# Kernel tuning notes

Hardware: AMD Instinct MI355X
Metric: run time of the kernel (lower is better)

Reference implementation:

```python
import jax, jax.numpy as jnp
import numpy as np

B, Q, S = 4, 256, 2048          # seqs, new query tokens per seq, total kv len per seq
H, KVH, D = 32, 8, 128          # query heads, kv heads (GQA), head dim
BLOCK = 16                      # paged-cache block size
NUM_BLOCKS = 640                # total blocks in the cache pool
BLOCKS_PER_SEQ = S // BLOCK     # 128


def setup_inputs() -> dict:
    key = jax.random.key(0)
    ks = jax.random.split(key, 5)
    T = B * Q
    q = jax.random.normal(ks[0], (T, H * D), jnp.float32)
    k = jax.random.normal(ks[1], (T, KVH * D), jnp.float32)
    v = jax.random.normal(ks[2], (T, KVH * D), jnp.float32)
    # pre-existing paged cache contents (context tokens already written)
    kv_cache = jax.random.normal(ks[3], (2, NUM_BLOCKS, BLOCK, KVH, D), jnp.float32)
    # assign blocks to sequences via a permutation (irregular block layout)
    perm = jax.random.permutation(ks[4], NUM_BLOCKS)[: B * BLOCKS_PER_SEQ]
    block_tables = perm.reshape(B, BLOCKS_PER_SEQ).astype(jnp.int32)
    # new tokens are the last Q positions of each sequence
    pos = jnp.arange(S - Q, S)
    slot_mapping = (block_tables[:, pos // BLOCK] * BLOCK + pos % BLOCK).reshape(-1).astype(jnp.int32)
    seq_lens = jnp.full((B,), S, jnp.int32)
    query_start_loc = (jnp.arange(B + 1) * Q).astype(jnp.int32)
    return dict(q=q, k=k, v=v, kv_cache=kv_cache, slot_mapping=slot_mapping,
                block_tables=block_tables, seq_lens=seq_lens, query_start_loc=query_start_loc)


def _paged_attention(q, k, v, kv_cache, slot_mapping, block_tables, seq_lens):
    T = q.shape[0]
    nB, _ = block_tables.shape
    _, _, block_size, kvh, d = kv_cache.shape
    h = q.shape[1] // d
    g = h // kvh                      # GQA group size
    qlen = T // nB                    # equal query lens (query_start_loc is uniform)
    scale = d ** -0.5
    # A) scatter new K/V into the flattened paged cache at slot_mapping
    kc = kv_cache[0].reshape(-1, kvh, d).at[slot_mapping].set(k.reshape(T, kvh, d))
    vc = kv_cache[1].reshape(-1, kvh, d).at[slot_mapping].set(v.reshape(T, kvh, d))
    # B) gather each sequence's kv via block_tables indirection  -> [B, S, KVH, D]
    slots = (block_tables[:, :, None] * block_size + jnp.arange(block_size)).reshape(nB, -1)
    k_seq = kc[slots]
    v_seq = vc[slots]
    s_kv = slots.shape[1]
    qh = q.reshape(nB, qlen, kvh, g, d)
    scores = jnp.einsum('bqkgd,bskd->bkgqs', qh, k_seq) * scale  # [B,KVH,G,Q,S]
    # causal mask: query qi sits at absolute pos seq_lens[b]-qlen+qi
    qpos = seq_lens[:, None] - qlen + jnp.arange(qlen)           # [B,Q]
    kpos = jnp.arange(s_kv)
    mask = (kpos[None, None, :] <= qpos[:, :, None]) & (kpos[None, None, :] < seq_lens[:, None, None])
    scores = jnp.where(mask[:, None, None], scores, -jnp.inf)
    p = jax.nn.softmax(scores, axis=-1)
    out = jnp.einsum('bkgqs,bskd->bqkgd', p, v_seq)              # [B,Q,KVH,G,D]
    return out.reshape(T, h * d)


def reference(q, k, v, kv_cache, slot_mapping, block_tables, seq_lens, query_start_loc):
    return _paged_attention(q, k, v, kv_cache, slot_mapping, block_tables, seq_lens)
```

## Files before the change

kernel.cpp:

```cpp
#include <hip/hip_runtime.h>

#define NUM_B 4
#define QLEN 256
#define SEQ 2048
#define NH 32
#define NKVH 8
#define HD 128
#define PAGE 16
#define NPAGES 640
#define PPS 128
#define KD (NKVH*HD)
#define VOFF ((size_t)NPAGES*PAGE*KD)
#define KVB 64
#define QSCALE 0.08838834764831845f

typedef __attribute__((ext_vector_type(8))) short bhalf8;
typedef __attribute__((ext_vector_type(4))) float floatx4;

__device__ __forceinline__ unsigned short f2bf(float f){
  union { float f; unsigned u; } x; x.f = f;
  unsigned r = x.u + 0x7fffu + ((x.u >> 16) & 1u);
  return (unsigned short)(r >> 16);
}

__device__ __forceinline__ bhalf8 pack8(const float* v){
  bhalf8 o;
  o[0]=(short)f2bf(v[0]); o[1]=(short)f2bf(v[1]);
  o[2]=(short)f2bf(v[2]); o[3]=(short)f2bf(v[3]);
  o[4]=(short)f2bf(v[4]); o[5]=(short)f2bf(v[5]);
  o[6]=(short)f2bf(v[6]); o[7]=(short)f2bf(v[7]);
  return o;
}

__global__ void scatter_kv(const float* __restrict__ k, const float* __restrict__ v,
                           float* __restrict__ cache, const int* __restrict__ slots){
  int t = blockIdx.x, tid = threadIdx.x;
  int slot = slots[t];
  float4 kq = *(const float4*)(k + (size_t)t*KD + tid*4);
  float4 vq = *(const float4*)(v + (size_t)t*KD + tid*4);
  *(float4*)(cache + (size_t)slot*KD + tid*4) = kq;
  *(float4*)(cache + VOFF + (size_t)slot*KD + tid*4) = vq;
}

__global__ __launch_bounds__(512)
void paged_attn(const float* __restrict__ qin, const float* __restrict__ cache,
                const int* __restrict__ btab, float* __restrict__ out){
  __shared__ unsigned short Ks[2*KVB*HD];
  __shared__ unsigned short Vt[2*HD*KVB];
  __shared__ unsigned short Ps[8*16*KVB];
  __shared__ int slotT[PPS];

  const int tid = threadIdx.x;
  const int w = tid>>6, l = tid&63, l16 = l&15, lg = l>>4;
  const int bid = blockIdx.x;
  const int b = bid>>6, kvh = (bid>>3)&7, rt = bid&7;
  const int qlo = (rt&1)<<7;
  const int h = kvh*4 + (rt>>1);

  if (tid < PPS) slotT[tid] = btab[b*PPS + tid]*PAGE;

  bhalf8 aq[4];
  {
    int qi = qlo + w*16 + l16;
    const float* qp = qin + (size_t)(b*QLEN+qi)*(NH*HD) + h*HD;
    #pragma unroll
    for (int kc=0;kc<4;kc++){
      float4 f0 = *(const float4*)(qp + kc*32 + lg*8);
      float4 f1 = *(const float4*)(qp + kc*32 + lg*8 + 4);
      float tmp[8] = {f0.x*QSCALE,f0.y*QSCALE,f0.z*QSCALE,f0.w*QSCALE,
                      f1.x*QSCALE,f1.y*QSCALE,f1.z*QSCALE,f1.w*QSCALE};
      aq[kc] = pack8(tmp);
    }
  }
  __syncthreads();

  float4 ka0,ka1,kb0,kb1;
  float va[8], vb[8];
  const int dchK = tid&15, sA = tid>>4;
  const int dV = tid&127, scV = tid>>7;

  auto LOAD = [&](int t){
    const int s0 = t*KVB;
    int pA = s0 + sA, pB = pA + 32;
    int slA = slotT[pA>>4] + (pA&15);
    int slB = slotT[pB>>4] + (pB&15);
    const float4* kpA = (const float4*)(cache + (size_t)slA*KD + kvh*HD + dchK*8);
    const float4* kpB = (const float4*)(cache + (size_t)slB*KD + kvh*HD + dchK*8);
    ka0 = kpA[0]; ka1 = kpA[1]; kb0 = kpB[0]; kb1 = kpB[1];
    int sb0 = scV*8, sb1 = sb0 + 32;
    const float* vp0 = cache + VOFF + (size_t)(slotT[(s0+sb0)>>4] + (sb0&15))*KD + kvh*HD + dV;
    const float* vp1 = cache + VOFF + (size_t)(slotT[(s0+sb1)>>4] + (sb1&15))*KD + kvh*HD + dV;
    #pragma unroll
    for (int i=0;i<8;i++){ va[i] = vp0[(size_t)i*KD]; vb[i] = vp1[(size_t)i*KD]; }
  };

  auto WRITE = [&](int buf){
    unsigned short* K_ = Ks + buf*(KVB*HD);
    unsigned short* V_ = Vt + buf*(HD*KVB);
    {
      float t0[8]={ka0.x,ka0.y,ka0.z,ka0.w,ka1.x,ka1.y,ka1.z,ka1.w};
      int off0 = sA*256 + dchK*16; off0 ^= (sA&7)<<4;
      *(bhalf8*)((char*)K_ + off0) = pack8(t0);
      float t1[8]={kb0.x,kb0.y,kb0.z,kb0.w,kb1.x,kb1.y,kb1.z,kb1.w};
      int sB = sA + 32;
      int off1 = sB*256 + dchK*16; off1 ^= (sB&7)<<4;
      *(bhalf8*)((char*)K_ + off1) = pack8(t1);
    }
    {
      int sb0 = scV*8, sb1 = sb0 + 32;
      int off0 = dV*(KVB*2) + sb0*2; off0 ^= (dV&7)<<4;
      *(bhalf8*)((char*)V_ + off0) = pack8(va);
      int off1 = dV*(KVB*2) + sb1*2; off1 ^= (dV&7)<<4;
      *(bhalf8*)((char*)V_ + off1) = pack8(vb);
    }
  };

  float mrun[4], lrun[4]; floatx4 acc[8];
  #pragma unroll
  for (int r=0;r<4;r++){ mrun[r]=-1e30f; lrun[r]=0.f; }
  #pragma unroll
  for (int dt=0;dt<8;dt++) acc[dt] = floatx4{0.f,0.f,0.f,0.f};

  const int nt = (qlo==0)?30:32;
  const int qpbase = SEQ - QLEN + qlo + w*16 + lg*4;
  unsigned short* Pw = Ps + w*(16*KVB);

  LOAD(0); WRITE(0);
  __syncthreads();
  int cur = 0;

  for (int t=0;t<nt;t++){
    const int s0 = t*KVB;
    const bool pre = (t+1 < nt);
    if (pre) LOAD(t+1);
    const unsigned short* K_ = Ks + cur*(KVB*HD);
    const unsigned short* V_ = Vt + cur*(HD*KVB);

    floatx4 S[4];
    #pragma unroll
    for (int st=0;st<4;st++){
      S[st] = floatx4{0.f,0.f,0.f,0.f};
      int srow = st*16 + l16;
      #pragma unroll
      for (int kc=0;kc<4;kc++){
        int off = srow*256 + (kc*32+lg*8)*2; off ^= (srow&7)<<4;
        bhalf8 bk = *(bhalf8*)((char*)K_ + off);
        S[st] = __builtin_amdgcn_mfma_f32_16x16x32_bf16(aq[kc], bk, S[st], 0,0,0);
      }
    }

    float pe[4][4];
    float alpha[4];
    const bool masked = (t >= nt-2);
    #pragma unroll
    for (int r=0;r<4;r++){
      float v0=S[0][r], v1=S[1][r], v2=S[2][r], v3=S[3][r];
      if (masked){
        int qp_ = qpbase + r;
        if (s0 +  0 + l16 > qp_) v0 = -1e30f;
        if (s0 + 16 + l16 > qp_) v1 = -1e30f;
        if (s0 + 32 + l16 > qp_) v2 = -1e30f;
        if (s0 + 48 + l16 > qp_) v3 = -1e30f;
      }
      float tm = fmaxf(fmaxf(v0,v1),fmaxf(v2,v3));
      #pragma unroll
      for (int dd=1; dd<16; dd<<=1) tm = fmaxf(tm, __shfl_xor(tm, dd));
      float mnew = fmaxf(mrun[r], tm);
      float al = __expf(mrun[r]-mnew);
      float e0=__expf(v0-mnew), e1=__expf(v1-mnew), e2=__expf(v2-mnew), e3=__expf(v3-mnew);
      pe[0][r]=e0; pe[1][r]=e1; pe[2][r]=e2; pe[3][r]=e3;
      float sm = e0+e1+e2+e3;
      #pragma unroll
      for (int dd=1; dd<16; dd<<=1) sm += __shfl_xor(sm, dd);
      lrun[r] = lrun[r]*al + sm;
      mrun[r] = mnew;
      alpha[r] = al;
    }
    bool needr = (alpha[0]<1.f)|(alpha[1]<1.f)|(alpha[2]<1.f)|(alpha[3]<1.f);
    if (__any(needr)){
      #pragma unroll
      for (int dt=0;dt<8;dt++)
        #pragma unroll
        for (int r=0;r<4;r++) acc[dt][r] *= alpha[r];
    }

    #pragma unroll
    for (int st=0;st<4;st++)
      #pragma unroll
      for (int r=0;r<4;r++){
        int row = lg*4 + r;
        int off = row*(KVB*2) + (st*16+l16)*2; off ^= (row&7)<<4;
        *(unsigned short*)((char*)Pw + off) = f2bf(pe[st][r]);
      }
    bhalf8 pa[2];
    #pragma unroll
    for (int kk=0;kk<2;kk++){
      int off = l16*(KVB*2) + (kk*32+lg*8)*2; off ^= (l16&7)<<4;
      pa[kk] = *(bhalf8*)((char*)Pw + off);
    }
    #pragma unroll
    for (int dt=0;dt<8;dt++){
      #pragma unroll
      for (int kk=0;kk<2;kk++){
        int dr = dt*16 + l16;
        int off = dr*(KVB*2) + (kk*32+lg*8)*2; off ^= (dr&7)<<4;
        bhalf8 bv = *(bhalf8*)((char*)V_ + off);
        acc[dt] = __builtin_amdgcn_mfma_f32_16x16x32_bf16(pa[kk], bv, acc[dt], 0,0,0);
      }
    }

    if (pre){
      WRITE(cur^1);
      __syncthreads();
    }
    cur ^= 1;
  }

  #pragma unroll
  for (int dt=0;dt<8;dt++){
    #pragma unroll
    for (int r=0;r<4;r++){
      int qi = qlo + w*16 + lg*4 + r;
      out[(size_t)(b*QLEN+qi)*(NH*HD) + h*HD + dt*16 + l16] = acc[dt][r] / lrun[r];
    }
  }
}

extern "C" void kernel_launch(void* const* d_in, const int* in_sizes, int n_in,
                              void* d_out, int out_size, void* d_ws, size_t ws_size,
                              hipStream_t stream) {
  const float* q = (const float*)d_in[0];
  const float* k = (const float*)d_in[1];
  const float* v = (const float*)d_in[2];
  float*       cache = (float*)d_in[3];
  const int*   slot_mapping = (const int*)d_in[4];
  const int*   block_tables = (const int*)d_in[5];
  float* out = (float*)d_out;

  scatter_kv<<<NUM_B*QLEN, 256, 0, stream>>>(k, v, cache, slot_mapping);
  paged_attn<<<NUM_B*NKVH*8, 512, 0, stream>>>(q, cache, block_tables, out);
}
```

Baseline: 254.2 us.

## Repack paged KV into contiguous swizzled bf16 tiles and DMA them into LDS

Adds a repack kernel that gathers each sequence's K/V, taking new tokens from k/v directly and everything else through the block table. It writes them as pre-swizzled bf16 tiles, K row-major and V transposed, into workspace. The attention kernel then streams those tiles with global_load_lds DMA instead of per-thread fp32 gathers plus in-register conversion. This removes the redundant per-head-group gathering and conversion (each KV panel was converted 8 times), at the cost of an extra kernel, a workspace round trip, and no longer updating the cache in place when the workspace is large enough.

```diff
diff --git a/kernel.cpp b/kernel.cpp
--- a/kernel.cpp
+++ b/kernel.cpp
@@ -12,6 +12,9 @@
 #define KD (NKVH*HD)
 #define VOFF ((size_t)NPAGES*PAGE*KD)
 #define KVB 64
+#define NTILES (SEQ/KVB)
+#define TILE_BYTES (KVB*HD*2)
+#define NEWBASE (SEQ-QLEN)
 #define QSCALE 0.08838834764831845f
 
 typedef __attribute__((ext_vector_type(8))) short bhalf8;
@@ -31,6 +34,229 @@
   o[6]=(short)f2bf(v[6]); o[7]=(short)f2bf(v[7]);
   return o;
 }
+
+__device__ __forceinline__ void dma16(const void* g, void* l){
+  __builtin_amdgcn_global_load_lds(
+      (const __attribute__((address_space(1))) unsigned int*)g,
+      (__attribute__((address_space(3))) unsigned int*)l, 16, 0, 0);
+}
+
+
+__global__ __launch_bounds__(256)
+void repack(const float* __restrict__ kin, const float* __restrict__ vin,
+            const float* __restrict__ cache, const int* __restrict__ btab,
+            unsigned short* __restrict__ KT, unsigned short* __restrict__ VT){
+  __shared__ float Sf[64*132];
+  const int tid = threadIdx.x;
+  const int bid = blockIdx.x;
+  const int b = bid>>8, kvh = (bid>>5)&7, t = bid&31;
+  const size_t tb = ((size_t)(b*NKVH + kvh)*NTILES + t)*TILE_BYTES;
+
+  #pragma unroll
+  for (int i=0;i<8;i++){
+    int idx = tid + i*256;
+    int row = idx>>5, c4 = idx&31;
+    int s_abs = t*64 + row;
+    const float* src;
+    if (s_abs >= NEWBASE){
+      int tok = b*QLEN + (s_abs - NEWBASE);
+      src = kin + (size_t)tok*KD + kvh*HD;
+    } else {
+      int slot = btab[b*PPS + (s_abs>>4)]*PAGE + (s_abs&15);
+      src = cache + (size_t)slot*KD + kvh*HD;
+    }
+    *(float4*)(Sf + row*132 + c4*4) = *(const float4*)(src + c4*4);
+  }
+  __syncthreads();
+  #pragma unroll
+  for (int j=0;j<4;j++){
+    int o = (tid + j*256)*16;
+    int sr = o>>8;
+    int d0 = ((o & 255) ^ ((sr&7)<<4))>>1;
+    const float* p = Sf + sr*132 + d0;
+    float tmp[8] = {p[0],p[1],p[2],p[3],p[4],p[5],p[6],p[7]};
+    *(bhalf8*)((char*)KT + tb + o) = pack8(tmp);
+  }
+  __syncthreads();
+
+  #pragma unroll
+  for (int i=0;i<8;i++){
+    int idx = tid + i*256;
+    int row = idx>>5, c4 = idx&31;
+    int s_abs = t*64 + row;
+    const float* src;
+    if (s_abs >= NEWBASE){
+      int tok = b*QLEN + (s_abs - NEWBASE);
+      src = vin + (size_t)tok*KD + kvh*HD;
+    } else {
+      int slot = btab[b*PPS + (s_abs>>4)]*PAGE + (s_abs&15);
+      src = cache + VOFF + (size_t)slot*KD + kvh*HD;
+    }
+    *(float4*)(Sf + row*132 + c4*4) = *(const float4*)(src + c4*4);
+  }
+  __syncthreads();
+  #pragma unroll
+  for (int j=0;j<4;j++){
+    int o = (tid + j*256)*16;
+    int d = o>>7;
+    int s0 = ((o & 127) ^ ((d&7)<<4))>>1;
+    float tmp[8];
+    #pragma unroll
+    for (int i2=0;i2<8;i2++) tmp[i2] = Sf[(s0+i2)*132 + d];
+    *(bhalf8*)((char*)VT + tb + o) = pack8(tmp);
+  }
+}
+
+__global__ __launch_bounds__(512)
+void attn_bf16(const float* __restrict__ qin,
+               const unsigned short* __restrict__ KT,
+               const unsigned short* __restrict__ VT,
+               float* __restrict__ out){
+  __shared__ unsigned short Ks[2*KVB*HD];
+  __shared__ unsigned short Vt[2*HD*KVB];
+  __shared__ unsigned short Ps[8*16*KVB];
+
+  const int tid = threadIdx.x;
+  const int w = tid>>6, l = tid&63, l16 = l&15, lg = l>>4;
+  const int bid = blockIdx.x;
+  const int b = bid>>6, kvh = (bid>>3)&7, rt = bid&7;
+  const int qlo = (rt&1)<<7;
+  const int h = kvh*4 + (rt>>1);
+  const size_t pan = (size_t)(b*NKVH + kvh)*NTILES;
+
+  bhalf8 aq[4];
+  {
+    int qi = qlo + w*16 + l16;
+    const float* qp = qin + (size_t)(b*QLEN+qi)*(NH*HD) + h*HD;
+    #pragma unroll
+    for (int kc=0;kc<4;kc++){
+      float4 f0 = *(const float4*)(qp + kc*32 + lg*8);
+      float4 f1 = *(const float4*)(qp + kc*32 + lg*8 + 4);
+      float tmp[8] = {f0.x*QSCALE,f0.y*QSCALE,f0.z*QSCALE,f0.w*QSCALE,
+                      f1.x*QSCALE,f1.y*QSCALE,f1.z*QSCALE,f1.w*QSCALE};
+      aq[kc] = pack8(tmp);
+    }
+  }
+
+  auto DMA = [&](int tk, int buf){
+    const char* gk = (const char*)KT + (pan+tk)*TILE_BYTES + w*2048 + (size_t)l*16;
+    const char* gv = (const char*)VT + (pan+tk)*TILE_BYTES + w*2048 + (size_t)l*16;
+    char* lk = (char*)Ks + buf*TILE_BYTES + w*2048;
+    char* lv = (char*)Vt + buf*TILE_BYTES + w*2048;
+    dma16(gk,        lk);
+    dma16(gk + 1024, lk + 1024);
+    dma16(gv,        lv);
+    dma16(gv + 1024, lv + 1024);
+  };
+
+  float mrun[4], lrun[4]; floatx4 acc[8];
+  #pragma unroll
+  for (int r=0;r<4;r++){ mrun[r]=-1e30f; lrun[r]=0.f; }
+  #pragma unroll
+  for (int dt=0;dt<8;dt++) acc[dt] = floatx4{0.f,0.f,0.f,0.f};
+
+  const int nt = (qlo==0)?30:32;
+  const int qpbase = SEQ - QLEN + qlo + w*16 + lg*4;
+  unsigned short* Pw = Ps + w*(16*KVB);
+
+  DMA(0, 0);
+  __syncthreads();
+  int cur = 0;
+
+  for (int t=0;t<nt;t++){
+    const int s0 = t*KVB;
+    const bool pre = (t+1 < nt);
+    if (pre) DMA(t+1, cur^1);
+    const unsigned short* K_ = Ks + cur*(KVB*HD);
+    const unsigned short* V_ = Vt + cur*(HD*KVB);
+
+    floatx4 S[4];
+    #pragma unroll
+    for (int st=0;st<4;st++){
+      S[st] = floatx4{0.f,0.f,0.f,0.f};
+      int srow = st*16 + l16;
+      #pragma unroll
+      for (int kc=0;kc<4;kc++){
+        int off = srow*256 + (kc*32+lg*8)*2; off ^= (srow&7)<<4;
+        bhalf8 bk = *(bhalf8*)((char*)K_ + off);
+        S[st] = __builtin_amdgcn_mfma_f32_16x16x32_bf16(aq[kc], bk, S[st], 0,0,0);
+      }
+    }
+
+    float pe[4][4];
+    float alpha[4];
+    const bool masked = (t >= nt-2);
+    #pragma unroll
+    for (int r=0;r<4;r++){
+      float v0=S[0][r], v1=S[1][r], v2=S[2][r], v3=S[3][r];
+      if (masked){
+        int qp_ = qpbase + r;
+        if (s0 +  0 + l16 > qp_) v0 = -1e30f;
+        if (s0 + 16 + l16 > qp_) v1 = -1e30f;
+        if (s0 + 32 + l16 > qp_) v2 = -1e30f;
+        if (s0 + 48 + l16 > qp_) v3 = -1e30f;
+      }
+      float tm = fmaxf(fmaxf(v0,v1),fmaxf(v2,v3));
+      #pragma unroll
+      for (int dd=1; dd<16; dd<<=1) tm = fmaxf(tm, __shfl_xor(tm, dd));
+      float mnew = fmaxf(mrun[r], tm);
+      float al = __expf(mrun[r]-mnew);
+      float e0=__expf(v0-mnew), e1=__expf(v1-mnew), e2=__expf(v2-mnew), e3=__expf(v3-mnew);
+      pe[0][r]=e0; pe[1][r]=e1; pe[2][r]=e2; pe[3][r]=e3;
+      float sm = e0+e1+e2+e3;
+      #pragma unroll
+      for (int dd=1; dd<16; dd<<=1) sm += __shfl_xor(sm, dd);
+      lrun[r] = lrun[r]*al + sm;
+      mrun[r] = mnew;
+      alpha[r] = al;
+    }
+    bool needr = (alpha[0]<1.f)|(alpha[1]<1.f)|(alpha[2]<1.f)|(alpha[3]<1.f);
+    if (__any(needr)){
+      #pragma unroll
+      for (int dt=0;dt<8;dt++)
+        #pragma unroll
+        for (int r=0;r<4;r++) acc[dt][r] *= alpha[r];
+    }
+
+    #pragma unroll
+    for (int st=0;st<4;st++)
+      #pragma unroll
+      for (int r=0;r<4;r++){
+        int row = lg*4 + r;
+        int off = row*(KVB*2) + (st*16+l16)*2; off ^= (row&7)<<4;
+        *(unsigned short*)((char*)Pw + off) = f2bf(pe[st][r]);
+      }
+    bhalf8 pa[2];
+    #pragma unroll
+    for (int kk=0;kk<2;kk++){
+      int off = l16*(KVB*2) + (kk*32+lg*8)*2; off ^= (l16&7)<<4;
+      pa[kk] = *(bhalf8*)((char*)Pw + off);
+    }
+    #pragma unroll
+    for (int dt=0;dt<8;dt++){
+      #pragma unroll
+      for (int kk=0;kk<2;kk++){
+        int dr = dt*16 + l16;
+        int off = dr*(KVB*2) + (kk*32+lg*8)*2; off ^= (dr&7)<<4;
+        bhalf8 bv = *(bhalf8*)((char*)V_ + off);
+        acc[dt] = __builtin_amdgcn_mfma_f32_16x16x32_bf16(pa[kk], bv, acc[dt], 0,0,0);
+      }
+    }
+
+    __syncthreads();
+    cur ^= 1;
+  }
+
+  #pragma unroll
+  for (int dt=0;dt<8;dt++){
+    #pragma unroll
+    for (int r=0;r<4;r++){
+      int qi = qlo + w*16 + lg*4 + r;
+      out[(size_t)(b*QLEN+qi)*(NH*HD) + h*HD + dt*16 + l16] = acc[dt][r] / lrun[r];
+    }
+  }
+}
+
 
 __global__ void scatter_kv(const float* __restrict__ k, const float* __restrict__ v,
                            float* __restrict__ cache, const int* __restrict__ slots){
@@ -237,6 +463,14 @@
   const int*   block_tables = (const int*)d_in[5];
   float* out = (float*)d_out;
 
-  scatter_kv<<<NUM_B*QLEN, 256, 0, stream>>>(k, v, cache, slot_mapping);
-  paged_attn<<<NUM_B*NKVH*8, 512, 0, stream>>>(q, cache, block_tables, out);
-}
+  const size_t need = (size_t)2 * NUM_B * NKVH * NTILES * TILE_BYTES;
+  if (ws_size >= need){
+    unsigned short* KT = (unsigned short*)d_ws;
+    unsigned short* VT = KT + (need/2)/2;
+    repack<<<NUM_B*NKVH*NTILES, 256, 0, stream>>>(k, v, cache, block_tables, KT, VT);
+    attn_bf16<<<NUM_B*NKVH*8, 512, 0, stream>>>(q, KT, VT, out);
+  } else {
+    scatter_kv<<<NUM_B*QLEN, 256, 0, stream>>>(k, v, cache, slot_mapping);
+    paged_attn<<<NUM_B*NKVH*8, 512, 0, stream>>>(q, cache, block_tables, out);
+  }
+}
```

Result: no change. 256.3 us (+0.8%).
